# Kernel tuning notes

Measured on AMD Instinct MI355X. Metric: run time of the kernel, lower is better.

The kernel has to match this reference:

```python
import jax, jax.numpy as jnp
import numpy as np

# ---- config (from DAREConfig init_kwargs) ----
TAU = 0.1
RHO_VIS = 0.5          # is_visual=True -> rho_target = rho_vis_target
PREFIX_KAPPA = 64
LAMBDA_RATIO = 1.0
LAMBDA_SOFT = 0.1
LAMBDA_HARD = 1.0

B, S = 256, 32768


def setup_inputs() -> dict:
    key = jax.random.key(0)
    k1, k2 = jax.random.split(key)
    importance = jax.random.normal(k1, (B, S), dtype=jnp.float32)
    modality_mask = jax.random.randint(k2, (B, S), 0, 2) > 0  # bool [B,S]
    return {"importance": importance, "modality_mask": modality_mask}


def reference(importance, modality_mask):
    """Vectorized DAREController.route(is_visual=True, training=True).

    The torch loop over batch with data-dependent k is replaced by a
    per-row k-th-largest threshold: for each row, k_b = min(int(rho*|mm_b|),
    |valid_b|); tokens with score >= k_b-th largest valid score are kept
    (this matches DifferentiableTopK's hard mask soft>0.5, i.e. exactly the
    top-k scores, assuming no ties).
    """
    mm = modality_mask.astype(bool)          # [B,S]
    b, s = importance.shape

    target = jnp.clip(mm.sum(axis=1).astype(jnp.float32) * RHO_VIS, 1.0)  # [B]
    prefix = jnp.arange(s) < min(PREFIX_KAPPA, s)                          # [S]
    eff = mm & ~prefix[None, :]                                            # [B,S] routable tokens
    n_valid = eff.sum(axis=1)                                              # [B]
    k = jnp.minimum(target.astype(jnp.int32), n_valid)                     # [B] per-row top-k size

    neg_inf = jnp.float32(-jnp.inf)
    masked = jnp.where(eff, importance, neg_inf)                           # [B,S]
    sorted_desc = -jnp.sort(-masked, axis=1)                               # [B,S]
    idx = jnp.clip(k - 1, 0, s - 1)                                        # [B]
    thresh = jnp.take_along_axis(sorted_desc, idx[:, None], axis=1)        # [B,1]
    hard = masked >= thresh                                                # top-k of valid tokens

    keep_mask = prefix[None, :] | (hard & (k > 0)[:, None])                # [B,S]

    # ---- training / is_visual losses ----
    kept = (keep_mask & mm).sum(axis=1).astype(jnp.float32)
    denom = mm.sum(axis=1).astype(jnp.float32) + 1e-6
    actual_ratio = kept / denom
    loss_ratio = jnp.mean(jnp.abs(actual_ratio - RHO_VIS))                 # F.l1_loss

    dropped = mm & ~keep_mask
    n_drop = dropped.sum()
    drop_mean = jnp.sum(jnp.where(dropped, importance, 0.0)) / jnp.maximum(n_drop, 1).astype(jnp.float32)
    loss_soft = jnp.where(n_drop > 0, drop_mean, 0.0)

    loss_hard = jnp.mean(jnp.clip(RHO_VIS - actual_ratio, 0.0))

    return (keep_mask,
            LAMBDA_RATIO * loss_ratio,
            LAMBDA_SOFT * loss_soft,
            LAMBDA_HARD * loss_hard)
```

## Files before the change

kernel.cpp:

```cpp
#include <hip/hip_runtime.h>


#define NB 256
#define NS 32768
#define KAPPA 64
#define NT 1024
#define V4 (NS / NT / 4)
#define NBIN 2048
#define NSEG 256
#define SEGW (NBIN / NSEG)

typedef float f32x4 __attribute__((ext_vector_type(4)));
typedef int   i32x4 __attribute__((ext_vector_type(4)));

__device__ __forceinline__ unsigned int fkey(float f) {
    unsigned int u = __float_as_uint(f);
    return (u & 0x80000000u) ? ~u : (u | 0x80000000u);
}

__device__ __forceinline__ float unkey(unsigned int k) {
    unsigned int u = (k & 0x80000000u) ? (k ^ 0x80000000u) : ~k;
    return __uint_as_float(u);
}

__global__ __launch_bounds__(NT) void dare_rows(const float* __restrict__ imp,
                                                const int* __restrict__ mask,
                                                float* __restrict__ keep,
                                                float* __restrict__ stats) {
    __shared__ unsigned int hist[NBIN];
    __shared__ unsigned int cand[NS];
    __shared__ unsigned int wtot[4];
    __shared__ unsigned int sh_mm, sh_eff, sh_cand;
    __shared__ unsigned int sh_b0, sh_rem, sh_thresh;
    __shared__ unsigned int sh_kept, sh_ndrop;
    __shared__ float sh_dsum;

    const int row = blockIdx.x;
    const int tid = threadIdx.x;
    const int lane = tid & 63;
    const int wid = tid >> 6;
    const f32x4* rimp4  = (const f32x4*)(imp  + (size_t)row * NS);
    const i32x4* rmask4 = (const i32x4*)(mask + (size_t)row * NS);
    f32x4*       rkeep4 = (f32x4*)      (keep + (size_t)row * NS);

    hist[tid] = 0;
    hist[tid + NT] = 0;
    if (tid == 0) {
        sh_mm = 0; sh_eff = 0; sh_cand = 0;
        sh_b0 = 0; sh_rem = 1; sh_thresh = 0;
        sh_kept = 0; sh_ndrop = 0; sh_dsum = 0.0f;
    }
    __syncthreads();

    unsigned int keys[V4 * 4];
    unsigned int effbits = 0, mmbits = 0;

    #pragma unroll
    for (int i = 0; i < V4; i++) {
        const int idx4 = tid + i * NT;
        const f32x4 v = rimp4[idx4];
        const i32x4 m = rmask4[idx4];
        #pragma unroll
        for (int j = 0; j < 4; j++) {
            const int e = i * 4 + j;
            const int col = idx4 * 4 + j;
            keys[e] = fkey(v[j]);
            const bool mm  = (m[j] != 0);
            const bool eff = mm && (col >= KAPPA);
            mmbits  |= (mm  ? 1u : 0u) << e;
            effbits |= (eff ? 1u : 0u) << e;
        }
    }

    #pragma unroll
    for (int e = 0; e < V4 * 4; e++) {
        if ((effbits >> e) & 1u) atomicAdd(&hist[keys[e] >> 21], 1u);
    }

    int mm_local  = __popc(mmbits);
    int eff_local = __popc(effbits);
    #pragma unroll
    for (int off = 32; off; off >>= 1) {
        mm_local  += __shfl_down(mm_local, off);
        eff_local += __shfl_down(eff_local, off);
    }
    if (lane == 0) {
        atomicAdd(&sh_mm,  (unsigned int)mm_local);
        atomicAdd(&sh_eff, (unsigned int)eff_local);
    }
    __syncthreads();

    unsigned int r[SEGW];
    unsigned int hsum = 0, s = 0;
    if (tid < NSEG) {
        #pragma unroll
        for (int b = 0; b < SEGW; b++) { r[b] = hist[tid * SEGW + b]; hsum += r[b]; }
        s = hsum;
        #pragma unroll
        for (int off = 1; off < 64; off <<= 1) {
            const unsigned int t = __shfl_down(s, off);
            if (lane + off < 64) s += t;
        }
        if (lane == 0) wtot[tid >> 6] = s;
    }
    __syncthreads();
    if (tid < NSEG) {
        unsigned int sfull = s;
        for (int w = (tid >> 6) + 1; w < 4; w++) sfull += wtot[w];
        const float target = fmaxf((float)sh_mm * 0.5f, 1.0f);
        const int k = min((int)target, (int)sh_eff);
        const unsigned int rem = (unsigned int)max(k, 1);
        const unsigned int above = sfull - hsum;
        if (sfull >= rem && above < rem) {
            unsigned int cum = above;
            #pragma unroll
            for (int b = SEGW - 1; b >= 0; b--) {
                if (cum + r[b] >= rem) { sh_b0 = tid * SEGW + b; sh_rem = rem - cum; break; }
                cum += r[b];
            }
        }
    }
    __syncthreads();

    const unsigned int b0 = sh_b0;
    const bool kpos = (sh_eff > 0);

    int kept_l = 0, ndrop_l = 0;
    float dsum_l = 0.0f;
    unsigned int defer = 0;

    #pragma unroll
    for (int i = 0; i < V4; i++) {
        const int idx4 = tid + i * NT;
        unsigned int cm = 0;
        #pragma unroll
        for (int j = 0; j < 4; j++) {
            const int e = i * 4 + j;
            const bool eff = (effbits >> e) & 1u;
            const bool is_cand = kpos && eff && ((keys[e] >> 21) == b0);
            cm |= (is_cand ? 1u : 0u) << j;
        }
        if (cm) {
            defer |= 1u << i;
            #pragma unroll
            for (int j = 0; j < 4; j++) {
                if ((cm >> j) & 1u) {
                    const unsigned int pos = atomicAdd(&sh_cand, 1u);
                    cand[pos] = keys[i * 4 + j];
                }
            }
        } else {
            f32x4 o;
            #pragma unroll
            for (int j = 0; j < 4; j++) {
                const int e = i * 4 + j;
                const int col = idx4 * 4 + j;
                const bool mm  = (mmbits >> e) & 1u;
                const bool eff = (effbits >> e) & 1u;
                const bool hard = kpos && eff && ((keys[e] >> 21) > b0);
                const bool kp = (col < KAPPA) || hard;
                o[j] = kp ? 1.0f : 0.0f;
                kept_l += (kp && mm) ? 1 : 0;
                const bool drop = mm && !kp;
                ndrop_l += drop ? 1 : 0;
                dsum_l += drop ? unkey(keys[e]) : 0.0f;
            }
            rkeep4[idx4] = o;
        }
    }
    __syncthreads();

    if (tid < 64) {
        const unsigned int cnt = sh_cand;
        if (cnt > 0) {
            unsigned int rem = sh_rem;
            unsigned int pref = 0;
            const int slots = (int)((cnt + 63u) >> 6);
            unsigned int lowreg[16];
            #pragma unroll
            for (int sl = 0; sl < 16; sl++) {
                const unsigned int idx = (unsigned int)lane + ((unsigned int)sl << 6);
                lowreg[sl] = (idx < cnt) ? (cand[idx] & 0x1FFFFFu) : 0xFFFFFFFFu;
            }
            for (int bit = 20; bit >= 0; bit--) {
                const unsigned int hi = pref >> (bit + 1);
                unsigned int cnt1 = 0;
                for (int sl = 0; sl < slots; sl++) {
                    unsigned int lw;
                    if (sl < 16) lw = lowreg[sl];
                    else {
                        const unsigned int idx = (unsigned int)lane + ((unsigned int)sl << 6);
                        lw = (idx < cnt) ? (cand[idx] & 0x1FFFFFu) : 0xFFFFFFFFu;
                    }
                    const bool m = (lw >> (bit + 1)) == hi && ((lw >> bit) & 1u);
                    cnt1 += (unsigned int)__popcll(__ballot(m));
                }
                if (cnt1 >= rem) pref |= 1u << bit; else rem -= cnt1;
            }
            if (lane == 0) sh_thresh = (b0 << 21) | pref;
        }
    }
    __syncthreads();

    const unsigned int thresh = sh_thresh;
    #pragma unroll
    for (int i = 0; i < V4; i++) {
        if ((defer >> i) & 1u) {
            const int idx4 = tid + i * NT;
            f32x4 o;
            #pragma unroll
            for (int j = 0; j < 4; j++) {
                const int e = i * 4 + j;
                const int col = idx4 * 4 + j;
                const bool mm  = (mmbits >> e) & 1u;
                const bool eff = (effbits >> e) & 1u;
                const bool hard = kpos && eff && (keys[e] >= thresh);
                const bool kp = (col < KAPPA) || hard;
                o[j] = kp ? 1.0f : 0.0f;
                kept_l += (kp && mm) ? 1 : 0;
                const bool drop = mm && !kp;
                ndrop_l += drop ? 1 : 0;
                dsum_l += drop ? unkey(keys[e]) : 0.0f;
            }
            rkeep4[idx4] = o;
        }
    }

    #pragma unroll
    for (int off = 32; off; off >>= 1) {
        kept_l  += __shfl_down(kept_l, off);
        ndrop_l += __shfl_down(ndrop_l, off);
        dsum_l  += __shfl_down(dsum_l, off);
    }
    if (lane == 0) {
        atomicAdd(&sh_kept,  (unsigned int)kept_l);
        atomicAdd(&sh_ndrop, (unsigned int)ndrop_l);
        atomicAdd(&sh_dsum,  dsum_l);
    }
    __syncthreads();
    if (tid == 0) {
        stats[row * 4 + 0] = (float)sh_kept;
        stats[row * 4 + 1] = (float)sh_mm;
        stats[row * 4 + 2] = (float)sh_ndrop;
        stats[row * 4 + 3] = sh_dsum;
    }
}

__global__ __launch_bounds__(256) void dare_losses(const float* __restrict__ stats,
                                                   float* __restrict__ out) {
    __shared__ float w_a[4], w_h[4], w_n[4], w_d[4];
    const int tid = threadIdx.x;
    const float kept = stats[tid * 4 + 0];
    const float mmc  = stats[tid * 4 + 1];
    const float nd   = stats[tid * 4 + 2];
    const float ds   = stats[tid * 4 + 3];
    const float ratio = kept / (mmc + 1e-6f);
    float a = fabsf(ratio - 0.5f);
    float h = fmaxf(0.5f - ratio, 0.0f);
    float n = nd, d = ds;
    #pragma unroll
    for (int off = 32; off; off >>= 1) {
        a += __shfl_down(a, off);
        h += __shfl_down(h, off);
        n += __shfl_down(n, off);
        d += __shfl_down(d, off);
    }
    const int wid = tid >> 6, lane = tid & 63;
    if (lane == 0) { w_a[wid] = a; w_h[wid] = h; w_n[wid] = n; w_d[wid] = d; }
    __syncthreads();
    if (tid == 0) {
        float sa = 0.f, shh = 0.f, sn = 0.f, sd = 0.f;
        for (int w = 0; w < 4; w++) { sa += w_a[w]; shh += w_h[w]; sn += w_n[w]; sd += w_d[w]; }
        out[0] = sa / (float)NB;
        out[1] = (sn > 0.0f) ? 0.1f * (sd / fmaxf(sn, 1.0f)) : 0.0f;
        out[2] = shh / (float)NB;
    }
}

extern "C" void kernel_launch(void* const* d_in, const int* in_sizes, int n_in,
                              void* d_out, int out_size, void* d_ws, size_t ws_size,
                              hipStream_t stream) {
    const float* imp  = (const float*)d_in[0];
    const int*   mask = (const int*)d_in[1];
    float* out   = (float*)d_out;
    float* stats = (float*)d_ws;

    dare_rows<<<NB, NT, 0, stream>>>(imp, mask, out, stats);
    dare_losses<<<1, 256, 0, stream>>>(stats, out + (size_t)NB * NS);
}
```

Measured before the change: 112.9 us.

## Replace candidate compaction and bitwise select with three-level radix histogram select

The single 2048-bin histogram, the candidate buffer and the one-wavefront bit-by-bit refinement are replaced by a three-pass radix select (11+11+10 bits) using shared histograms. Every element is then written once in a single output pass. The first-level histogram is split into four per-wave copies to reduce atomic contention, and loads and stores now use nontemporal hints. The aim is to remove the serial single-wave refinement and the 128KB candidate array, which should also help occupancy. The cost is two extra register passes over the keys and additional barriers.

```diff
diff --git a/kernel.cpp b/kernel.cpp
--- a/kernel.cpp
+++ b/kernel.cpp
@@ -6,9 +6,12 @@
 #define KAPPA 64
 #define NT 1024
 #define V4 (NS / NT / 4)
-#define NBIN 2048
+#define NCOPY 4
+#define NBIN0 2048
+#define PAD0 8
+#define NBIN1 2048
+#define NBIN2 1024
 #define NSEG 256
-#define SEGW (NBIN / NSEG)
 
 typedef float f32x4 __attribute__((ext_vector_type(4)));
 typedef int   i32x4 __attribute__((ext_vector_type(4)));
@@ -21,17 +24,49 @@
 __device__ __forceinline__ float unkey(unsigned int k) {
     unsigned int u = (k & 0x80000000u) ? (k ^ 0x80000000u) : ~k;
     return __uint_as_float(u);
+}
+
+template <int SEGW>
+__device__ __forceinline__ void scan_find(const unsigned int (&r)[SEGW], unsigned int hsum,
+                                          unsigned int rem, unsigned int* wtot,
+                                          unsigned int* out_bin, unsigned int* out_rem,
+                                          const int tid, const int lane, const int wid) {
+    unsigned int s = 0;
+    if (tid < NSEG) {
+        s = hsum;
+        #pragma unroll
+        for (int off = 1; off < 64; off <<= 1) {
+            const unsigned int t = __shfl_down(s, off);
+            if (lane + off < 64) s += t;
+        }
+        if (lane == 0) wtot[wid] = s;
+    }
+    __syncthreads();
+    if (tid < NSEG) {
+        unsigned int sfull = s;
+        for (int w = wid + 1; w < 4; w++) sfull += wtot[w];
+        const unsigned int above = sfull - hsum;
+        if (sfull >= rem && above < rem) {
+            unsigned int cum = above;
+            #pragma unroll
+            for (int b = SEGW - 1; b >= 0; b--) {
+                if (cum + r[b] >= rem) { *out_bin = (unsigned int)(tid * SEGW + b); *out_rem = rem - cum; break; }
+                cum += r[b];
+            }
+        }
+    }
 }
 
 __global__ __launch_bounds__(NT) void dare_rows(const float* __restrict__ imp,
                                                 const int* __restrict__ mask,
                                                 float* __restrict__ keep,
                                                 float* __restrict__ stats) {
-    __shared__ unsigned int hist[NBIN];
-    __shared__ unsigned int cand[NS];
+    __shared__ unsigned int hist0[NCOPY][NBIN0 + PAD0];
+    __shared__ unsigned int hist1[NBIN1];
+    __shared__ unsigned int hist2[NBIN2];
     __shared__ unsigned int wtot[4];
-    __shared__ unsigned int sh_mm, sh_eff, sh_cand;
-    __shared__ unsigned int sh_b0, sh_rem, sh_thresh;
+    __shared__ unsigned int sh_mm, sh_eff;
+    __shared__ unsigned int sh_b0, sh_rem0, sh_b1, sh_rem1, sh_thresh;
     __shared__ unsigned int sh_kept, sh_ndrop;
     __shared__ float sh_dsum;
 
@@ -43,23 +78,26 @@
     const i32x4* rmask4 = (const i32x4*)(mask + (size_t)row * NS);
     f32x4*       rkeep4 = (f32x4*)      (keep + (size_t)row * NS);
 
-    hist[tid] = 0;
-    hist[tid + NT] = 0;
+    #pragma unroll
+    for (int c = 0; c < NCOPY; c++) { hist0[c][tid] = 0; hist0[c][tid + NT] = 0; }
+    hist1[tid] = 0; hist1[tid + NT] = 0;
+    hist2[tid] = 0;
     if (tid == 0) {
-        sh_mm = 0; sh_eff = 0; sh_cand = 0;
-        sh_b0 = 0; sh_rem = 1; sh_thresh = 0;
+        sh_mm = 0; sh_eff = 0;
+        sh_b0 = 0; sh_rem0 = 1; sh_b1 = 0; sh_rem1 = 1; sh_thresh = 0;
         sh_kept = 0; sh_ndrop = 0; sh_dsum = 0.0f;
     }
     __syncthreads();
 
     unsigned int keys[V4 * 4];
     unsigned int effbits = 0, mmbits = 0;
+    const int hc = wid & (NCOPY - 1);
 
     #pragma unroll
     for (int i = 0; i < V4; i++) {
         const int idx4 = tid + i * NT;
-        const f32x4 v = rimp4[idx4];
-        const i32x4 m = rmask4[idx4];
+        const f32x4 v = __builtin_nontemporal_load(&rimp4[idx4]);
+        const i32x4 m = __builtin_nontemporal_load(&rmask4[idx4]);
         #pragma unroll
         for (int j = 0; j < 4; j++) {
             const int e = i * 4 + j;
@@ -71,10 +109,9 @@
             effbits |= (eff ? 1u : 0u) << e;
         }
     }
-
     #pragma unroll
     for (int e = 0; e < V4 * 4; e++) {
-        if ((effbits >> e) & 1u) atomicAdd(&hist[keys[e] >> 21], 1u);
+        if ((effbits >> e) & 1u) atomicAdd(&hist0[hc][keys[e] >> 21], 1u);
     }
 
     int mm_local  = __popc(mmbits);
@@ -90,140 +127,94 @@
     }
     __syncthreads();
 
-    unsigned int r[SEGW];
-    unsigned int hsum = 0, s = 0;
-    if (tid < NSEG) {
-        #pragma unroll
-        for (int b = 0; b < SEGW; b++) { r[b] = hist[tid * SEGW + b]; hsum += r[b]; }
-        s = hsum;
-        #pragma unroll
-        for (int off = 1; off < 64; off <<= 1) {
-            const unsigned int t = __shfl_down(s, off);
-            if (lane + off < 64) s += t;
-        }
-        if (lane == 0) wtot[tid >> 6] = s;
-    }
-    __syncthreads();
-    if (tid < NSEG) {
-        unsigned int sfull = s;
-        for (int w = (tid >> 6) + 1; w < 4; w++) sfull += wtot[w];
+    {
+        unsigned int r0[NBIN0 / NSEG] = {};
+        unsigned int hsum = 0;
+        if (tid < NSEG) {
+            #pragma unroll
+            for (int b = 0; b < NBIN0 / NSEG; b++) {
+                unsigned int v = 0;
+                #pragma unroll
+                for (int c = 0; c < NCOPY; c++) v += hist0[c][tid * (NBIN0 / NSEG) + b];
+                r0[b] = v; hsum += v;
+            }
+        }
         const float target = fmaxf((float)sh_mm * 0.5f, 1.0f);
         const int k = min((int)target, (int)sh_eff);
         const unsigned int rem = (unsigned int)max(k, 1);
-        const unsigned int above = sfull - hsum;
-        if (sfull >= rem && above < rem) {
-            unsigned int cum = above;
-            #pragma unroll
-            for (int b = SEGW - 1; b >= 0; b--) {
-                if (cum + r[b] >= rem) { sh_b0 = tid * SEGW + b; sh_rem = rem - cum; break; }
-                cum += r[b];
-            }
-        }
+        scan_find<NBIN0 / NSEG>(r0, hsum, rem, wtot, &sh_b0, &sh_rem0, tid, lane, wid);
     }
     __syncthreads();
 
     const unsigned int b0 = sh_b0;
+    #pragma unroll
+    for (int e = 0; e < V4 * 4; e++) {
+        if (((effbits >> e) & 1u) && (keys[e] >> 21) == b0)
+            atomicAdd(&hist1[(keys[e] >> 10) & (NBIN1 - 1)], 1u);
+    }
+    __syncthreads();
+    {
+        unsigned int r1[NBIN1 / NSEG] = {};
+        unsigned int hsum = 0;
+        if (tid < NSEG) {
+            #pragma unroll
+            for (int b = 0; b < NBIN1 / NSEG; b++) {
+                const unsigned int v = hist1[tid * (NBIN1 / NSEG) + b];
+                r1[b] = v; hsum += v;
+            }
+        }
+        scan_find<NBIN1 / NSEG>(r1, hsum, sh_rem0, wtot, &sh_b1, &sh_rem1, tid, lane, wid);
+    }
+    __syncthreads();
+
+    const unsigned int b1 = sh_b1;
+    const unsigned int top22 = (b0 << 11) | b1;
+    #pragma unroll
+    for (int e = 0; e < V4 * 4; e++) {
+        if (((effbits >> e) & 1u) && (keys[e] >> 10) == top22)
+            atomicAdd(&hist2[keys[e] & (NBIN2 - 1)], 1u);
+    }
+    __syncthreads();
+    {
+        unsigned int r2[NBIN2 / NSEG] = {};
+        unsigned int hsum = 0;
+        if (tid < NSEG) {
+            #pragma unroll
+            for (int b = 0; b < NBIN2 / NSEG; b++) {
+                const unsigned int v = hist2[tid * (NBIN2 / NSEG) + b];
+                r2[b] = v; hsum += v;
+            }
+        }
+        unsigned int dummy_rem;
+        scan_find<NBIN2 / NSEG>(r2, hsum, sh_rem1, wtot, &sh_thresh, &dummy_rem, tid, lane, wid);
+    }
+    __syncthreads();
+
+    const unsigned int thresh = (top22 << 10) | sh_thresh;
     const bool kpos = (sh_eff > 0);
 
     int kept_l = 0, ndrop_l = 0;
     float dsum_l = 0.0f;
-    unsigned int defer = 0;
 
     #pragma unroll
     for (int i = 0; i < V4; i++) {
         const int idx4 = tid + i * NT;
-        unsigned int cm = 0;
+        f32x4 o;
         #pragma unroll
         for (int j = 0; j < 4; j++) {
             const int e = i * 4 + j;
+            const int col = idx4 * 4 + j;
+            const bool mm  = (mmbits >> e) & 1u;
             const bool eff = (effbits >> e) & 1u;
-            const bool is_cand = kpos && eff && ((keys[e] >> 21) == b0);
-            cm |= (is_cand ? 1u : 0u) << j;
-        }
-        if (cm) {
-            defer |= 1u << i;
-            #pragma unroll
-            for (int j = 0; j < 4; j++) {
-                if ((cm >> j) & 1u) {
-                    const unsigned int pos = atomicAdd(&sh_cand, 1u);
-                    cand[pos] = keys[i * 4 + j];
-                }
-            }
-        } else {
-            f32x4 o;
-            #pragma unroll
-            for (int j = 0; j < 4; j++) {
-                const int e = i * 4 + j;
-                const int col = idx4 * 4 + j;
-                const bool mm  = (mmbits >> e) & 1u;
-                const bool eff = (effbits >> e) & 1u;
-                const bool hard = kpos && eff && ((keys[e] >> 21) > b0);
-                const bool kp = (col < KAPPA) || hard;
-                o[j] = kp ? 1.0f : 0.0f;
-                kept_l += (kp && mm) ? 1 : 0;
-                const bool drop = mm && !kp;
-                ndrop_l += drop ? 1 : 0;
-                dsum_l += drop ? unkey(keys[e]) : 0.0f;
-            }
-            rkeep4[idx4] = o;
-        }
-    }
-    __syncthreads();
-
-    if (tid < 64) {
-        const unsigned int cnt = sh_cand;
-        if (cnt > 0) {
-            unsigned int rem = sh_rem;
-            unsigned int pref = 0;
-            const int slots = (int)((cnt + 63u) >> 6);
-            unsigned int lowreg[16];
-            #pragma unroll
-            for (int sl = 0; sl < 16; sl++) {
-                const unsigned int idx = (unsigned int)lane + ((unsigned int)sl << 6);
-                lowreg[sl] = (idx < cnt) ? (cand[idx] & 0x1FFFFFu) : 0xFFFFFFFFu;
-            }
-            for (int bit = 20; bit >= 0; bit--) {
-                const unsigned int hi = pref >> (bit + 1);
-                unsigned int cnt1 = 0;
-                for (int sl = 0; sl < slots; sl++) {
-                    unsigned int lw;
-                    if (sl < 16) lw = lowreg[sl];
-                    else {
-                        const unsigned int idx = (unsigned int)lane + ((unsigned int)sl << 6);
-                        lw = (idx < cnt) ? (cand[idx] & 0x1FFFFFu) : 0xFFFFFFFFu;
-                    }
-                    const bool m = (lw >> (bit + 1)) == hi && ((lw >> bit) & 1u);
-                    cnt1 += (unsigned int)__popcll(__ballot(m));
-                }
-                if (cnt1 >= rem) pref |= 1u << bit; else rem -= cnt1;
-            }
-            if (lane == 0) sh_thresh = (b0 << 21) | pref;
-        }
-    }
-    __syncthreads();
-
-    const unsigned int thresh = sh_thresh;
-    #pragma unroll
-    for (int i = 0; i < V4; i++) {
-        if ((defer >> i) & 1u) {
-            const int idx4 = tid + i * NT;
-            f32x4 o;
-            #pragma unroll
-            for (int j = 0; j < 4; j++) {
-                const int e = i * 4 + j;
-                const int col = idx4 * 4 + j;
-                const bool mm  = (mmbits >> e) & 1u;
-                const bool eff = (effbits >> e) & 1u;
-                const bool hard = kpos && eff && (keys[e] >= thresh);
-                const bool kp = (col < KAPPA) || hard;
-                o[j] = kp ? 1.0f : 0.0f;
-                kept_l += (kp && mm) ? 1 : 0;
-                const bool drop = mm && !kp;
-                ndrop_l += drop ? 1 : 0;
-                dsum_l += drop ? unkey(keys[e]) : 0.0f;
-            }
-            rkeep4[idx4] = o;
-        }
+            const bool hard = kpos && eff && (keys[e] >= thresh);
+            const bool kp = (col < KAPPA) || hard;
+            o[j] = kp ? 1.0f : 0.0f;
+            kept_l += (kp && mm) ? 1 : 0;
+            const bool drop = mm && !kp;
+            ndrop_l += drop ? 1 : 0;
+            dsum_l += drop ? unkey(keys[e]) : 0.0f;
+        }
+        __builtin_nontemporal_store(o, &rkeep4[idx4]);
     }
 
     #pragma unroll
```

Result: no change. 115.1 us (+2.0%).
